# Kernel tuning notes

Measured on AMD Instinct MI355X. Metric: run time of the kernel, lower is better.

Reference implementation:

```python
import jax, jax.numpy as jnp
import numpy as np

T, B, I = 2048, 256, 64
H = 1280          # hidden_size = 20 * input_size
H4 = H // 4       # fc2 out / LSTMCell input = 320
H8 = H // 8       # LSTMCell hidden = 160
O = 32            # output_size


def setup_inputs() -> dict:
    key = jax.random.key(0)
    ks = jax.random.split(key, 12)
    n = lambda k, shape, fan: jax.random.normal(k, shape, jnp.float32) * (1.0 / np.sqrt(fan))
    return {
        "inputs": jax.random.normal(ks[0], (T, B, I), jnp.float32),
        "W1": n(ks[1], (H, I), I),
        "b1": jnp.zeros((H,), jnp.float32),
        "W2": n(ks[2], (H4, H), H),
        "b2": jnp.zeros((H4,), jnp.float32),
        "W_ih": n(ks[3], (4 * H8, H4), H4),
        "W_hh": n(ks[4], (4 * H8, H8), H8),
        "b_ih": jnp.zeros((4 * H8,), jnp.float32),
        "b_hh": jnp.zeros((4 * H8,), jnp.float32),
        "W3": n(ks[5], (O, H8), H8),
        "b3": jnp.zeros((O,), jnp.float32),
    }


def reference(inputs, W1, b1, W2, b2, W_ih, W_hh, b_ih, b_hh, W3, b3):
    # Eval-mode forward: dropout / noise are identity when not training.
    Bd = inputs.shape[1]
    Hc = W_hh.shape[1]

    def step(carry, x_t):
        h, c = carry
        x = jax.nn.leaky_relu(x_t @ W1.T + b1)          # [B, H]
        x = jax.nn.leaky_relu(x @ W2.T + b2)            # [B, H//4]
        gates = x @ W_ih.T + b_ih + h @ W_hh.T + b_hh   # [B, 4*H//8]
        i, f, g, o = jnp.split(gates, 4, axis=-1)       # PyTorch gate order i,f,g,o
        i = jax.nn.sigmoid(i)
        f = jax.nn.sigmoid(f)
        g = jnp.tanh(g)
        o = jax.nn.sigmoid(o)
        c = f * c + i * g
        h = o * jnp.tanh(c)
        y = h @ W3.T + b3                                # [B, O]
        return (h, c), y

    h0 = jnp.zeros((Bd, Hc), inputs.dtype)
    c0 = jnp.zeros((Bd, Hc), inputs.dtype)
    _, ys = jax.lax.scan(step, (h0, c0), inputs)         # [T, B, O]
    return ys
```

## Files before the change

### kernel.cpp

```cpp
#include <hip/hip_runtime.h>
#include <hip/hip_bf16.h>

#define T_STEPS 2048
#define BATCH   256
#define INW     64
#define H1      1280
#define H4D     320
#define H8D     160
#define G4      640
#define ONUM    32

typedef __attribute__((ext_vector_type(8))) short short8;
typedef __attribute__((ext_vector_type(4))) float floatx4;
typedef __hip_bfloat16 bf16;

union frag8 { short8 v; uint2 u2[2]; };

__device__ __forceinline__ float b2f(bf16 v) { return __bfloat162float(v); }
__device__ __forceinline__ bf16  f2b(float v) { return __float2bfloat16(v); }
__device__ __forceinline__ float bfu(unsigned short u) { return __uint_as_float((unsigned)u << 16); }
__device__ __forceinline__ float fsig(float x)  { return __fdividef(1.0f, 1.0f + __expf(-x)); }
__device__ __forceinline__ float ftanh(float x) { return __fdividef(2.0f, 1.0f + __expf(-2.0f * x)) - 1.0f; }

__device__ __forceinline__ void lds_barrier() {
  asm volatile("s_waitcnt lgkmcnt(0)\n\ts_barrier" ::: "memory");
}

struct bf16x4 { bf16 a, b, c, d; };
__global__ void cast_f32_bf16_v4(const float* __restrict__ s, bf16* __restrict__ d, int n4) {
  int i = blockIdx.x * blockDim.x + threadIdx.x;
  if (i >= n4) return;
  float4 v = reinterpret_cast<const float4*>(s)[i];
  bf16x4 o{f2b(v.x), f2b(v.y), f2b(v.z), f2b(v.w)};
  reinterpret_cast<bf16x4*>(d)[i] = o;
}

__global__ void cast_permute_wih(const float* __restrict__ s, bf16* __restrict__ d) {
  int i = blockIdx.x * blockDim.x + threadIdx.x;
  if (i >= G4 * (H4D / 4)) return;
  int p = i / (H4D / 4), k4 = (i - p * (H4D / 4)) * 4;
  int g = p & 3, ix = p >> 2;
  float4 v = *reinterpret_cast<const float4*>(&s[(size_t)(g * 160 + ix) * H4D + k4]);
  bf16x4 o{f2b(v.x), f2b(v.y), f2b(v.z), f2b(v.w)};
  *reinterpret_cast<bf16x4*>(&d[(size_t)p * H4D + k4]) = o;
}

#define SMEM_BYTES 65024

__device__ void fused_gemm(char* smem, int tid, int gb,
    const bf16* __restrict__ Xg, const bf16* __restrict__ W1g, const float* __restrict__ b1v,
    const bf16* __restrict__ W2g, const float* __restrict__ b2v,
    const bf16* __restrict__ Wpg, const float* __restrict__ bihv, const float* __restrict__ bhhv,
    bf16* __restrict__ gxw)
{
  bf16 (*Y1s)[72]  = reinterpret_cast<bf16 (*)[72]>(smem);
  bf16 (*W2cs)[72] = reinterpret_cast<bf16 (*)[72]>(smem + 9216);
  const int lane = tid & 63, wave = tid >> 6;
  const int mrow = lane & 15, quad = lane >> 4;
  const int wm = (wave >= 5) ? 1 : 0;
  const int wn = wave - wm * 5;
  const int fm = wave & 3;
  const int fnp = (wave >> 2) & 1;
  const size_t R0 = (size_t)gb * 64;

  short8 xf0, xf1;
  if (wave < 8) {
    const bf16* xrow = Xg + (R0 + fm * 16 + mrow) * INW;
    xf0 = *reinterpret_cast<const short8*>(xrow + quad * 8);
    xf1 = *reinterpret_cast<const short8*>(xrow + 32 + quad * 8);
  }

  short8 w1f[4];
  if (wave < 8) {
    const bf16* wr0 = W1g + (size_t)((fnp * 2 + 0) * 16 + mrow) * INW;
    const bf16* wr1 = W1g + (size_t)((fnp * 2 + 1) * 16 + mrow) * INW;
    w1f[0] = *reinterpret_cast<const short8*>(wr0 + quad * 8);
    w1f[1] = *reinterpret_cast<const short8*>(wr0 + 32 + quad * 8);
    w1f[2] = *reinterpret_cast<const short8*>(wr1 + quad * 8);
    w1f[3] = *reinterpret_cast<const short8*>(wr1 + 32 + quad * 8);
  }

  short8 w2r[4];
#pragma unroll
  for (int i = 0; i < 4; ++i) {
    int v = tid + i * 640;
    w2r[i] = *reinterpret_cast<const short8*>(&W2g[(size_t)(v >> 3) * H1 + (v & 7) * 8]);
  }
#pragma unroll
  for (int i = 0; i < 4; ++i) {
    int v = tid + i * 640;
    *reinterpret_cast<short8*>(&W2cs[v >> 3][(v & 7) * 8]) = w2r[i];
  }

  floatx4 acc2[2][4] = {};

  for (int c = 0; c < 20; ++c) {
    if (wave < 8) {
      floatx4 a10 = {}, a11 = {};
      a10 = __builtin_amdgcn_mfma_f32_16x16x32_bf16(xf0, w1f[0], a10, 0, 0, 0);
      a10 = __builtin_amdgcn_mfma_f32_16x16x32_bf16(xf1, w1f[1], a10, 0, 0, 0);
      a11 = __builtin_amdgcn_mfma_f32_16x16x32_bf16(xf0, w1f[2], a11, 0, 0, 0);
      a11 = __builtin_amdgcn_mfma_f32_16x16x32_bf16(xf1, w1f[3], a11, 0, 0, 0);
      if (c < 19) {
        const bf16* wr0 = W1g + (size_t)((c + 1) * 64 + (fnp * 2 + 0) * 16 + mrow) * INW;
        const bf16* wr1 = W1g + (size_t)((c + 1) * 64 + (fnp * 2 + 1) * 16 + mrow) * INW;
        w1f[0] = *reinterpret_cast<const short8*>(wr0 + quad * 8);
        w1f[1] = *reinterpret_cast<const short8*>(wr0 + 32 + quad * 8);
        w1f[2] = *reinterpret_cast<const short8*>(wr1 + quad * 8);
        w1f[3] = *reinterpret_cast<const short8*>(wr1 + 32 + quad * 8);
      }
#pragma unroll
      for (int r = 0; r < 4; ++r) {
        int row = fm * 16 + quad * 4 + r;
        {
          int col = (fnp * 2 + 0) * 16 + mrow;
          float vv = a10[r] + b1v[c * 64 + col];
          Y1s[row][col] = f2b(vv > 0.0f ? vv : 0.01f * vv);
        }
        {
          int col = (fnp * 2 + 1) * 16 + mrow;
          float vv = a11[r] + b1v[c * 64 + col];
          Y1s[row][col] = f2b(vv > 0.0f ? vv : 0.01f * vv);
        }
      }
    }
    if (c < 19) {
#pragma unroll
      for (int i = 0; i < 4; ++i) {
        int v = tid + i * 640;
        w2r[i] = *reinterpret_cast<const short8*>(
            &W2g[(size_t)(v >> 3) * H1 + (c + 1) * 64 + (v & 7) * 8]);
      }
    }
    lds_barrier();
#pragma unroll
    for (int kk = 0; kk < 2; ++kk) {
      short8 af0 = *reinterpret_cast<const short8*>(&Y1s[wm * 32 + mrow][kk * 32 + quad * 8]);
      short8 af1 = *reinterpret_cast<const short8*>(&Y1s[wm * 32 + 16 + mrow][kk * 32 + quad * 8]);
#pragma unroll
      for (int j = 0; j < 4; ++j) {
        short8 bfj = *reinterpret_cast<const short8*>(
            &W2cs[wn * 64 + j * 16 + mrow][kk * 32 + quad * 8]);
        acc2[0][j] = __builtin_amdgcn_mfma_f32_16x16x32_bf16(af0, bfj, acc2[0][j], 0, 0, 0);
        acc2[1][j] = __builtin_amdgcn_mfma_f32_16x16x32_bf16(af1, bfj, acc2[1][j], 0, 0, 0);
      }
    }
    lds_barrier();
    if (c < 19) {
#pragma unroll
      for (int i = 0; i < 4; ++i) {
        int v = tid + i * 640;
        *reinterpret_cast<short8*>(&W2cs[v >> 3][(v & 7) * 8]) = w2r[i];
      }
    }
  }

  bf16 (*Y2s)[328] = reinterpret_cast<bf16 (*)[328]>(smem);
  char* Wps = smem + 41984;
  short8 wpr[2];
#pragma unroll
  for (int i = 0; i < 2; ++i) {
    int v = tid + i * 640;
    wpr[i] = *reinterpret_cast<const short8*>(&Wpg[(size_t)(v >> 2) * H4D + (v & 3) * 8]);
  }
#pragma unroll
  for (int i = 0; i < 2; ++i) {
#pragma unroll
    for (int j = 0; j < 4; ++j) {
      int col = wn * 64 + j * 16 + mrow;
      float bb = b2v[col];
#pragma unroll
      for (int r = 0; r < 4; ++r) {
        int row = wm * 32 + i * 16 + quad * 4 + r;
        float vv = acc2[i][j][r] + bb;
        Y2s[row][col] = f2b(vv > 0.0f ? vv : 0.01f * vv);
      }
    }
  }
#pragma unroll
  for (int i = 0; i < 2; ++i) {
    int v = tid + i * 640;
    frag8 u; u.v = wpr[i];
    char* p = Wps + (size_t)(v >> 2) * 72 + (v & 3) * 16;
    *reinterpret_cast<uint2*>(p) = u.u2[0];
    *reinterpret_cast<uint2*>(p + 8) = u.u2[1];
  }
  lds_barrier();

  floatx4 ag[2][4];
  for (int t = 0; t < 20; ++t) {
    int h = t / 10, kc = t - h * 10;
    if (kc == 0) {
#pragma unroll
      for (int i = 0; i < 2; ++i)
#pragma unroll
        for (int j = 0; j < 4; ++j) ag[i][j] = (floatx4){0.f, 0.f, 0.f, 0.f};
    }
    short8 af0 = *reinterpret_cast<const short8*>(&Y2s[wm * 32 + mrow][kc * 32 + quad * 8]);
    short8 af1 = *reinterpret_cast<const short8*>(&Y2s[wm * 32 + 16 + mrow][kc * 32 + quad * 8]);
    frag8 bfj[4];
#pragma unroll
    for (int j = 0; j < 4; ++j) {
      const char* p = Wps + (size_t)(wn * 64 + j * 16 + mrow) * 72 + quad * 16;
      bfj[j].u2[0] = *reinterpret_cast<const uint2*>(p);
      bfj[j].u2[1] = *reinterpret_cast<const uint2*>(p + 8);
    }
#pragma unroll
    for (int j = 0; j < 4; ++j) {
      ag[0][j] = __builtin_amdgcn_mfma_f32_16x16x32_bf16(af0, bfj[j].v, ag[0][j], 0, 0, 0);
      ag[1][j] = __builtin_amdgcn_mfma_f32_16x16x32_bf16(af1, bfj[j].v, ag[1][j], 0, 0, 0);
    }
    if (t < 19) {
      int nh = (t + 1) / 10, nk = (t + 1) - nh * 10;
#pragma unroll
      for (int i = 0; i < 2; ++i) {
        int v = tid + i * 640;
        wpr[i] = *reinterpret_cast<const short8*>(
            &Wpg[(size_t)(nh * 320 + (v >> 2)) * H4D + nk * 32 + (v & 3) * 8]);
      }
    }
    lds_barrier();
    if (t < 19) {
#pragma unroll
      for (int i = 0; i < 2; ++i) {
        int v = tid + i * 640;
        frag8 u; u.v = wpr[i];
        char* p = Wps + (size_t)(v >> 2) * 72 + (v & 3) * 16;
        *reinterpret_cast<uint2*>(p) = u.u2[0];
        *reinterpret_cast<uint2*>(p + 8) = u.u2[1];
      }
    }
    lds_barrier();
    if (kc == 9) {
#pragma unroll
      for (int j = 0; j < 4; ++j) {
        int p = h * 320 + wn * 64 + j * 16 + mrow;
        int g = p & 3, ix = p >> 2;
        float bb = bihv[g * 160 + ix] + bhhv[g * 160 + ix];
#pragma unroll
        for (int i = 0; i < 2; ++i)
#pragma unroll
          for (int r = 0; r < 4; ++r) {
            int row = wm * 32 + i * 16 + quad * 4 + r;
            gxw[(R0 + row) * 640 + p] = f2b(ag[i][j][r] + bb);
          }
      }
    }
  }
}

__device__ void recur_path(char* smem, int tid, int bid,
    const bf16* __restrict__ gx, const bf16* __restrict__ Whh,
    bf16* __restrict__ h_ws, float* __restrict__ c_ws,
    bf16* __restrict__ hh, int Tc, int init)
{
  bf16 (*hbuf)[16][168] = reinterpret_cast<bf16 (*)[16][168]>(smem);
  const int lane = tid & 63;
  const int wave = tid >> 6;
  const int mrow = lane & 15;
  const int quad = lane >> 4;
  const int bbase = bid * 4;
  const int ixg = wave * 16 + mrow;

  short8 whf[4][5];
#pragma unroll
  for (int g = 0; g < 4; ++g)
#pragma unroll
    for (int ks = 0; ks < 5; ++ks)
      whf[g][ks] = *reinterpret_cast<const short8*>(
          &Whh[(size_t)(g * 160 + ixg) * 160 + ks * 32 + quad * 8]);

  for (int e = tid; e < 2 * 16 * 168; e += 640)
    reinterpret_cast<bf16*>(hbuf)[e] = f2b(0.0f);
  __syncthreads();
  {
    int r = tid / 160, cix = tid - r * 160;
    hbuf[0][r * 4][cix] = init ? f2b(0.0f) : h_ws[(size_t)(bbase + r) * 160 + cix];
  }
  float c0 = init ? 0.0f : c_ws[(size_t)(bbase + quad) * 160 + ixg];
  __syncthreads();

  const uint2* __restrict__ gxp = reinterpret_cast<const uint2*>(gx);
  const size_t goff = (size_t)(bbase + quad) * 160 + ixg;

  auto body = [&](int t, int rb, uint2 g) {
    short8 af[5];
#pragma unroll
    for (int ks = 0; ks < 5; ++ks)
      af[ks] = *reinterpret_cast<const short8*>(&hbuf[rb][mrow][ks * 32 + quad * 8]);
    floatx4 acc[4] = {};
#pragma unroll
    for (int ks = 0; ks < 5; ++ks)
#pragma unroll
      for (int g4 = 0; g4 < 4; ++g4)
        acc[g4] = __builtin_amdgcn_mfma_f32_16x16x32_bf16(af[ks], whf[g4][ks], acc[g4], 0, 0, 0);
    union { uint2 u; unsigned short s[4]; } q;
    q.u = g;
    float xi = acc[0][0] + bfu(q.s[0]);
    float xf = acc[1][0] + bfu(q.s[1]);
    float xg = acc[2][0] + bfu(q.s[2]);
    float xo = acc[3][0] + bfu(q.s[3]);
    float iv = fsig(xi), fv = fsig(xf), gvv = ftanh(xg), ov = fsig(xo);
    c0 = fv * c0 + iv * gvv;
    bf16 hv = f2b(ov * ftanh(c0));
    hbuf[rb ^ 1][quad * 4][ixg] = hv;
    hh[((size_t)t * 256 + bbase + quad) * 160 + ixg] = hv;
  };

  uint2 g0 = gxp[goff];
  uint2 g1 = gxp[(size_t)(256 * 160) + goff];
  for (int t = 0; t < Tc; t += 2) {
    body(t, 0, g0);
    if (t + 2 < Tc) g0 = gxp[(size_t)(t + 2) * (256 * 160) + goff];
    lds_barrier();
    body(t + 1, 1, g1);
    if (t + 3 < Tc) g1 = gxp[(size_t)(t + 3) * (256 * 160) + goff];
    lds_barrier();
  }

  {
    int r = tid / 160, cix = tid - r * 160;
    h_ws[(size_t)(bbase + r) * 160 + cix] = hbuf[0][r * 4][cix];
  }
  c_ws[(size_t)(bbase + quad) * 160 + ixg] = c0;
}

__device__ void ygemm(int tid, int yb, const bf16* __restrict__ hh,
                      const bf16* __restrict__ W3w, const float* __restrict__ b3,
                      float* __restrict__ outy)
{
  const int lane = tid & 63, wave = tid >> 6;
  if (wave >= 8) return;
  const int mrow = lane & 15, quad = lane >> 4;
  const size_t R0 = (size_t)yb * 128 + wave * 16;
  short8 af[5], bf0[5], bf1[5];
#pragma unroll
  for (int ks = 0; ks < 5; ++ks) {
    af[ks]  = *reinterpret_cast<const short8*>(&hh[(R0 + mrow) * 160 + ks * 32 + quad * 8]);
    bf0[ks] = *reinterpret_cast<const short8*>(&W3w[(size_t)mrow * 160 + ks * 32 + quad * 8]);
    bf1[ks] = *reinterpret_cast<const short8*>(&W3w[(size_t)(16 + mrow) * 160 + ks * 32 + quad * 8]);
  }
  floatx4 a0 = {}, a1 = {};
#pragma unroll
  for (int ks = 0; ks < 5; ++ks) {
    a0 = __builtin_amdgcn_mfma_f32_16x16x32_bf16(af[ks], bf0[ks], a0, 0, 0, 0);
    a1 = __builtin_amdgcn_mfma_f32_16x16x32_bf16(af[ks], bf1[ks], a1, 0, 0, 0);
  }
  float bb0 = b3[mrow], bb1 = b3[16 + mrow];
#pragma unroll
  for (int r = 0; r < 4; ++r) {
    size_t row = R0 + quad * 4 + r;
    outy[row * 32 + mrow] = a0[r] + bb0;
    outy[row * 32 + 16 + mrow] = a1[r] + bb1;
  }
}

__global__ __launch_bounds__(640, 1) void fused_step(
    int has_recur, const bf16* gxr, const bf16* Whh,
    bf16* h_ws, float* c_ws, bf16* hh_w, int Tc, int init,
    int nbg, const bf16* Xc, const bf16* W1w, const float* b1v,
    const bf16* W2w, const float* b2v, const bf16* Wpw,
    const float* bihv, const float* bhhv, bf16* gxw,
    int has_y, const bf16* hh_r, const bf16* W3w, const float* b3, float* outy)
{
  __shared__ __align__(16) char smem[SMEM_BYTES];
  const int tid = threadIdx.x;
  if (blockIdx.x < 64) {
    if (has_recur)
      recur_path(smem, tid, blockIdx.x, gxr, Whh, h_ws, c_ws, hh_w, Tc, init);
    return;
  }
  int gb = blockIdx.x - 64;
  if (gb < nbg) {
    fused_gemm(smem, tid, gb, Xc, W1w, b1v, W2w, b2v, Wpw, bihv, bhhv, gxw);
    return;
  }
  if (has_y)
    ygemm(tid, gb - nbg, hh_r, W3w, b3, outy);
}

extern "C" void kernel_launch(void* const* d_in, const int* in_sizes, int n_in,
                              void* d_out, int out_size, void* d_ws, size_t ws_size,
                              hipStream_t stream)
{
  const float* inp = (const float*)d_in[0];
  const float* W1  = (const float*)d_in[1];
  const float* b1  = (const float*)d_in[2];
  const float* W2  = (const float*)d_in[3];
  const float* b2  = (const float*)d_in[4];
  const float* Wih = (const float*)d_in[5];
  const float* Whh = (const float*)d_in[6];
  const float* bih = (const float*)d_in[7];
  const float* bhh = (const float*)d_in[8];
  const float* W3  = (const float*)d_in[9];
  const float* b3  = (const float*)d_in[10];
  float* out = (float*)d_out;

  char* ws = (char*)d_ws;
  size_t off = 0;
  auto alloc = [&](size_t bytes) -> char* {
    char* p = ws + off;
    off += (bytes + 255) & ~(size_t)255;
    return p;
  };

  bf16* inpb = (bf16*)alloc((size_t)T_STEPS * BATCH * INW * 2);
  bf16* w1b  = (bf16*)alloc((size_t)H1 * INW * 2);
  bf16* w2b  = (bf16*)alloc((size_t)H4D * H1 * 2);
  bf16* wpb  = (bf16*)alloc((size_t)G4 * H4D * 2);
  bf16* whhb = (bf16*)alloc((size_t)G4 * H8D * 2);
  bf16* w3b  = (bf16*)alloc((size_t)ONUM * H8D * 2);
  bf16* h_ws = (bf16*)alloc((size_t)BATCH * H8D * 2);
  float* c_ws = (float*)alloc((size_t)BATCH * H8D * 4);
  size_t fixed = off;

  int Tc = 128;
  while (Tc > 16) {
    size_t Mc = (size_t)Tc * BATCH;
    size_t need = fixed
      + 2 * ((Mc * G4 * 2 + 255) & ~(size_t)255)
      + 2 * ((Mc * H8D * 2 + 255) & ~(size_t)255);
    if (need <= ws_size) break;
    Tc >>= 1;
  }
  const size_t Mc = (size_t)Tc * BATCH;
  bf16* gxb[2], *hhb[2];
  for (int i = 0; i < 2; ++i) gxb[i] = (bf16*)alloc(Mc * G4 * 2);
  for (int i = 0; i < 2; ++i) hhb[i] = (bf16*)alloc(Mc * H8D * 2);

  {
    int n4 = T_STEPS * BATCH * INW / 4;
    cast_f32_bf16_v4<<<(n4 + 255) / 256, 256, 0, stream>>>(inp, inpb, n4);
    n4 = H1 * INW / 4;
    cast_f32_bf16_v4<<<(n4 + 255) / 256, 256, 0, stream>>>(W1, w1b, n4);
    n4 = H4D * H1 / 4;
    cast_f32_bf16_v4<<<(n4 + 255) / 256, 256, 0, stream>>>(W2, w2b, n4);
    int np = G4 * (H4D / 4);
    cast_permute_wih<<<(np + 255) / 256, 256, 0, stream>>>(Wih, wpb);
    n4 = G4 * H8D / 4;
    cast_f32_bf16_v4<<<(n4 + 255) / 256, 256, 0, stream>>>(Whh, whhb, n4);
    n4 = ONUM * H8D / 4;
    cast_f32_bf16_v4<<<(n4 + 255) / 256, 256, 0, stream>>>(W3, w3b, n4);
  }

  const int nch = T_STEPS / Tc;
  const int nGB = (int)(Mc / 64);
  const int nYB = (int)(Mc / 128);

  for (int L = 0; L <= nch + 1; ++L) {
    const int hg = (L < nch) ? 1 : 0;
    const int hr = (L >= 1 && L <= nch) ? 1 : 0;
    const int hy = (L >= 2) ? 1 : 0;
    const int cg = L, cr = L - 1, cy = L - 2;

    const bf16* Xc = inpb + (size_t)(hg ? cg : 0) * Mc * INW;
    bf16* gxw = gxb[cg & 1];
    const bf16* gxr = gxb[(hr ? cr : 0) & 1];
    bf16* hh_w = hhb[(hr ? cr : 0) & 1];
    const bf16* hh_r = hhb[(hy ? cy : 0) & 1];
    float* outy = out + (size_t)(hy ? cy : 0) * Tc * BATCH * ONUM;
    const int nbg = hg ? nGB : 0;
    const int nby = hy ? nYB : 0;

    fused_step<<<64 + nbg + nby, 640, 0, stream>>>(
        hr, gxr, whhb, h_ws, c_ws, hh_w, Tc, (cr == 0) ? 1 : 0,
        nbg, Xc, w1b, b1, w2b, b2, wpb, bih, bhh, gxw,
        hy, hh_r, w3b, b3, outy);
  }
}
```

Baseline: 2.764 ms.

## Pack 16 batch rows per recurrence block using full MFMA M dimension

Each recurrence block now processes 16 batch rows instead of 4, so all rows of the 16x16 MFMA output carry real data rather than padding. The recurrence uses 16 blocks instead of 64, which frees compute units for the concurrent GEMM blocks. Each lane now runs the gate nonlinearities for 4 rows per step, so the serial per-step latency grows, with more gate loads and more hidden-state stores per lane.

```diff
diff --git a/kernel.cpp b/kernel.cpp
--- a/kernel.cpp
+++ b/kernel.cpp
@@ -259,7 +259,7 @@
   const int wave = tid >> 6;
   const int mrow = lane & 15;
   const int quad = lane >> 4;
-  const int bbase = bid * 4;
+  const int bbase = bid * 16;
   const int ixg = wave * 16 + mrow;
 
   short8 whf[4][5];
@@ -270,20 +270,29 @@
       whf[g][ks] = *reinterpret_cast<const short8*>(
           &Whh[(size_t)(g * 160 + ixg) * 160 + ks * 32 + quad * 8]);
 
-  for (int e = tid; e < 2 * 16 * 168; e += 640)
-    reinterpret_cast<bf16*>(hbuf)[e] = f2b(0.0f);
+  for (int e = tid; e < 16 * 160; e += 640) {
+    int r = e / 160, cix = e - r * 160;
+    hbuf[0][r][cix] = init ? f2b(0.0f) : h_ws[(size_t)(bbase + r) * 160 + cix];
+  }
+  float c0[4];
+#pragma unroll
+  for (int r = 0; r < 4; ++r)
+    c0[r] = init ? 0.0f : c_ws[(size_t)(bbase + quad * 4 + r) * 160 + ixg];
   __syncthreads();
-  {
-    int r = tid / 160, cix = tid - r * 160;
-    hbuf[0][r * 4][cix] = init ? f2b(0.0f) : h_ws[(size_t)(bbase + r) * 160 + cix];
-  }
-  float c0 = init ? 0.0f : c_ws[(size_t)(bbase + quad) * 160 + ixg];
-  __syncthreads();
 
   const uint2* __restrict__ gxp = reinterpret_cast<const uint2*>(gx);
-  const size_t goff = (size_t)(bbase + quad) * 160 + ixg;
-
-  auto body = [&](int t, int rb, uint2 g) {
+  size_t goff[4];
+#pragma unroll
+  for (int r = 0; r < 4; ++r)
+    goff[r] = (size_t)(bbase + quad * 4 + r) * 160 + ixg;
+
+  uint2 gA[4], gB[4];
+#pragma unroll
+  for (int r = 0; r < 4; ++r) gA[r] = gxp[goff[r]];
+#pragma unroll
+  for (int r = 0; r < 4; ++r) gB[r] = gxp[(size_t)(256 * 160) + goff[r]];
+
+  auto body = [&](int t, int rb, uint2 (&g)[4]) {
     short8 af[5];
 #pragma unroll
     for (int ks = 0; ks < 5; ++ks)
@@ -294,35 +303,44 @@
 #pragma unroll
       for (int g4 = 0; g4 < 4; ++g4)
         acc[g4] = __builtin_amdgcn_mfma_f32_16x16x32_bf16(af[ks], whf[g4][ks], acc[g4], 0, 0, 0);
-    union { uint2 u; unsigned short s[4]; } q;
-    q.u = g;
-    float xi = acc[0][0] + bfu(q.s[0]);
-    float xf = acc[1][0] + bfu(q.s[1]);
-    float xg = acc[2][0] + bfu(q.s[2]);
-    float xo = acc[3][0] + bfu(q.s[3]);
-    float iv = fsig(xi), fv = fsig(xf), gvv = ftanh(xg), ov = fsig(xo);
-    c0 = fv * c0 + iv * gvv;
-    bf16 hv = f2b(ov * ftanh(c0));
-    hbuf[rb ^ 1][quad * 4][ixg] = hv;
-    hh[((size_t)t * 256 + bbase + quad) * 160 + ixg] = hv;
+#pragma unroll
+    for (int r = 0; r < 4; ++r) {
+      union { uint2 u; unsigned short s[4]; } q;
+      q.u = g[r];
+      float xi = acc[0][r] + bfu(q.s[0]);
+      float xf = acc[1][r] + bfu(q.s[1]);
+      float xg = acc[2][r] + bfu(q.s[2]);
+      float xo = acc[3][r] + bfu(q.s[3]);
+      float iv = fsig(xi), fv = fsig(xf), gvv = ftanh(xg), ov = fsig(xo);
+      c0[r] = fv * c0[r] + iv * gvv;
+      bf16 hv = f2b(ov * ftanh(c0[r]));
+      hbuf[rb ^ 1][quad * 4 + r][ixg] = hv;
+      hh[((size_t)t * 256 + bbase + quad * 4 + r) * 160 + ixg] = hv;
+    }
   };
 
-  uint2 g0 = gxp[goff];
-  uint2 g1 = gxp[(size_t)(256 * 160) + goff];
   for (int t = 0; t < Tc; t += 2) {
-    body(t, 0, g0);
-    if (t + 2 < Tc) g0 = gxp[(size_t)(t + 2) * (256 * 160) + goff];
-    lds_barrier();
-    body(t + 1, 1, g1);
-    if (t + 3 < Tc) g1 = gxp[(size_t)(t + 3) * (256 * 160) + goff];
-    lds_barrier();
-  }
-
-  {
-    int r = tid / 160, cix = tid - r * 160;
-    h_ws[(size_t)(bbase + r) * 160 + cix] = hbuf[0][r * 4][cix];
-  }
-  c_ws[(size_t)(bbase + quad) * 160 + ixg] = c0;
+    body(t, 0, gA);
+    if (t + 2 < Tc) {
+#pragma unroll
+      for (int r = 0; r < 4; ++r) gA[r] = gxp[(size_t)(t + 2) * (256 * 160) + goff[r]];
+    }
+    lds_barrier();
+    body(t + 1, 1, gB);
+    if (t + 3 < Tc) {
+#pragma unroll
+      for (int r = 0; r < 4; ++r) gB[r] = gxp[(size_t)(t + 3) * (256 * 160) + goff[r]];
+    }
+    lds_barrier();
+  }
+
+  for (int e = tid; e < 16 * 160; e += 640) {
+    int r = e / 160, cix = e - r * 160;
+    h_ws[(size_t)(bbase + r) * 160 + cix] = hbuf[0][r][cix];
+  }
+#pragma unroll
+  for (int r = 0; r < 4; ++r)
+    c_ws[(size_t)(bbase + quad * 4 + r) * 160 + ixg] = c0[r];
 }
 
 __device__ void ygemm(int tid, int yb, const bf16* __restrict__ hh,
@@ -365,12 +383,12 @@
 {
   __shared__ __align__(16) char smem[SMEM_BYTES];
   const int tid = threadIdx.x;
-  if (blockIdx.x < 64) {
+  if (blockIdx.x < 16) {
     if (has_recur)
       recur_path(smem, tid, blockIdx.x, gxr, Whh, h_ws, c_ws, hh_w, Tc, init);
     return;
   }
-  int gb = blockIdx.x - 64;
+  int gb = blockIdx.x - 16;
   if (gb < nbg) {
     fused_gemm(smem, tid, gb, Xc, W1w, b1v, W2w, b2v, Wpw, bihv, bhhv, gxw);
     return;
@@ -462,7 +480,7 @@
     const int nbg = hg ? nGB : 0;
     const int nby = hy ? nYB : 0;
 
-    fused_step<<<64 + nbg + nby, 640, 0, stream>>>(
+    fused_step<<<16 + nbg + nby, 640, 0, stream>>>(
         hr, gxr, whhb, h_ws, c_ws, hh_w, Tc, (cr == 0) ? 1 : 0,
         nbg, Xc, w1b, b1, w2b, b2, wpb, bih, bhh, gxw,
         hy, hh_r, w3b, b3, outy);
```

New measurement: 5.113 ms. 1.85x slower.
